# Performance work log

Hardware: AMD Instinct MI355X
Metric: run time of the kernel (lower is better)

## Reference

```python
import jax, jax.numpy as jnp
import numpy as np

D_MODEL = 1024
NUM_HEADS = 16
HEAD_DIM = D_MODEL // NUM_HEADS
B, S = 4, 2048


def setup_inputs() -> dict:
    key = jax.random.key(0)
    ks = jax.random.split(key, 11)
    scale = 1.0 / np.sqrt(D_MODEL)
    inp = {
        "query": jax.random.normal(ks[0], (B, S, D_MODEL), dtype=jnp.float32),
        "key": jax.random.normal(ks[1], (B, S, D_MODEL), dtype=jnp.float32),
        "value": jax.random.normal(ks[2], (B, S, D_MODEL), dtype=jnp.float32),
        "Wq": jax.random.normal(ks[3], (D_MODEL, D_MODEL), dtype=jnp.float32) * scale,
        "bq": jnp.zeros((D_MODEL,), dtype=jnp.float32),
        "Wk": jax.random.normal(ks[4], (D_MODEL, D_MODEL), dtype=jnp.float32) * scale,
        "bk": jnp.zeros((D_MODEL,), dtype=jnp.float32),
        "Wv": jax.random.normal(ks[5], (D_MODEL, D_MODEL), dtype=jnp.float32) * scale,
        "bv": jnp.zeros((D_MODEL,), dtype=jnp.float32),
        "Wo": jax.random.normal(ks[6], (D_MODEL, D_MODEL), dtype=jnp.float32) * scale,
        "bo": jnpp.zeros((D_MODEL,), dtype=jnp.float32) if False else jnp.zeros((D_MODEL,), dtype=jnp.float32),
    }
    return inp


def reference(query, key, value, Wq, bq, Wk, bk, Wv, bv, Wo, bo):
    # Linear projections (torch Linear: x @ W.T + b), split into heads: [B,H,S,Dh]
    def split_heads(x):
        b, s, _ = x.shape
        return x.reshape(b, s, NUM_HEADS, HEAD_DIM).transpose(0, 2, 1, 3)

    q = split_heads(query @ Wq.T + bq)
    k = split_heads(key @ Wk.T + bk)
    v = split_heads(value @ Wv.T + bv)

    # Explicit attention: [B,H,S,S] scores, softmax, AV
    scores = jnp.einsum("bhqd,bhkd->bhqk", q, k) / np.sqrt(HEAD_DIM).astype(np.float32)
    attn = jax.nn.softmax(scores, axis=-1)
    ctx = jnp.einsum("bhqk,bhkd->bhqd", attn, v)

    # Merge heads and output projection
    b = ctx.shape[0]
    ctx = ctx.transpose(0, 2, 1, 3).reshape(b, -1, D_MODEL)
    return ctx @ Wo.T + bo
```

## Files before the change

### kernel.cpp

```cpp
#include <hip/hip_runtime.h>
#include <stdint.h>

#define DMODEL 1024
#define NHEADS 16
#define HDIM   64
#define BB     4
#define SS     2048
#define MM     (BB*SS)
#define QKV_ELEMS ((size_t)8388608)

typedef unsigned short ushort_t;
typedef __bf16    bf16x8  __attribute__((ext_vector_type(8)));
typedef _Float16  half4   __attribute__((ext_vector_type(4)));
typedef _Float16  half2_t __attribute__((ext_vector_type(2)));
typedef float     floatx4 __attribute__((ext_vector_type(4)));

__device__ inline ushort_t f32_to_bf16(float f) {
    union { float f; uint32_t u; } v; v.f = f;
    uint32_t r = v.u + 0x7FFF + ((v.u >> 16) & 1);
    return (ushort_t)(r >> 16);
}
__device__ inline ushort_t f32_to_f16u(float f) {
    union { _Float16 h; ushort_t u; } v; v.h = (_Float16)f; return v.u;
}
__device__ inline half2_t pkrtz(float a, float b) {
    return __builtin_bit_cast(half2_t, __builtin_amdgcn_cvt_pkrtz(a, b));
}
__device__ inline void glds16(const void* g, void* l) {
    __builtin_amdgcn_global_load_lds(
        (const __attribute__((address_space(1))) unsigned int*)g,
        (__attribute__((address_space(3))) unsigned int*)l, 16, 0, 0);
}

__global__ __launch_bounds__(256) void convert_bf16(const float* __restrict__ in,
                                                    ushort_t* __restrict__ out) {
    size_t i = ((size_t)blockIdx.x * 256 + threadIdx.x) * 8;
    float4 a = *(const float4*)&in[i];
    float4 b = *(const float4*)&in[i + 4];
    ushort_t t[8];
    t[0] = f32_to_bf16(a.x); t[1] = f32_to_bf16(a.y);
    t[2] = f32_to_bf16(a.z); t[3] = f32_to_bf16(a.w);
    t[4] = f32_to_bf16(b.x); t[5] = f32_to_bf16(b.y);
    t[6] = f32_to_bf16(b.z); t[7] = f32_to_bf16(b.w);
    *(uint4*)&out[i] = *(uint4*)t;
}

__global__ __launch_bounds__(256) void convert_w3(
    const float* __restrict__ w0, const float* __restrict__ w1, const float* __restrict__ w2,
    ushort_t* __restrict__ o0, ushort_t* __restrict__ o1, ushort_t* __restrict__ o2) {
    const float* src = (blockIdx.y == 0) ? w0 : (blockIdx.y == 1) ? w1 : w2;
    ushort_t*    dst = (blockIdx.y == 0) ? o0 : (blockIdx.y == 1) ? o1 : o2;
    size_t i = ((size_t)blockIdx.x * 256 + threadIdx.x) * 8;
    float4 a = *(const float4*)&src[i];
    float4 b = *(const float4*)&src[i + 4];
    ushort_t t[8];
    t[0] = f32_to_bf16(a.x); t[1] = f32_to_bf16(a.y);
    t[2] = f32_to_bf16(a.z); t[3] = f32_to_bf16(a.w);
    t[4] = f32_to_bf16(b.x); t[5] = f32_to_bf16(b.y);
    t[6] = f32_to_bf16(b.z); t[7] = f32_to_bf16(b.w);
    *(uint4*)&dst[i] = *(uint4*)t;
}

template<int OUT>
__global__ __launch_bounds__(256) void gemm_bf16(
    const ushort_t* __restrict__ A, const ushort_t* __restrict__ W,
    const float* __restrict__ bias, void* __restrict__ O, float scale)
{
    __shared__ ushort_t As[3 * 4096];
    __shared__ ushort_t Bs[3 * 4096];

    const int tid  = threadIdx.x;
    const int lane = tid & 63;
    const int quad = lane >> 4;
    const int l15  = lane & 15;
    const int wid  = tid >> 6;
    const int wr   = wid >> 1, wc = wid & 1;

    const int bid = blockIdx.x;
    const int n0  = ((bid >> 3) & 7) * 128;
    const int m0  = ((bid & 7) + ((bid >> 6) << 3)) * 128;

    floatx4 acc[4][4];
    #pragma unroll
    for (int i = 0; i < 4; i++)
        #pragma unroll
        for (int j = 0; j < 4; j++)
            acc[i][j] = (floatx4){0.f, 0.f, 0.f, 0.f};

    auto stage = [&](int kk, int bufB) {
        #pragma unroll
        for (int j = 0; j < 2; j++) {
            const int p  = tid + j * 256;
            const int ph = p << 4;
            const int lg = ph ^ (((ph >> 7) & 7) << 4);
            const int row = lg >> 6, cc = (lg >> 4) & 3;
            glds16(&A[(size_t)(m0 + row) * DMODEL + kk + cc * 8], (char*)As + bufB + ph);
            glds16(&W[(size_t)(n0 + row) * DMODEL + kk + cc * 8], (char*)Bs + bufB + ph);
        }
    };

    stage(0, 0);
    stage(32, 8192);

    int cbB = 0;
    for (int k0 = 0; k0 < DMODEL; k0 += 32) {
        if (k0 + 32 < DMODEL) asm volatile("s_waitcnt vmcnt(4)" ::: "memory");
        else                  asm volatile("s_waitcnt vmcnt(0)" ::: "memory");
        __builtin_amdgcn_s_barrier();
        __builtin_amdgcn_sched_barrier(0);
        const int k2 = k0 + 64;
        if (k2 < DMODEL) {
            int nbB = cbB + 16384; if (nbB >= 24576) nbB -= 24576;
            stage(k2, nbB);
        }
        bf16x8 af[4], bfv[4];
        #pragma unroll
        for (int i = 0; i < 4; i++) {
            const int r = wr * 64 + i * 16 + l15;
            const int L = (r << 6) | (quad << 4);
            af[i] = *(const bf16x8*)((const char*)As + cbB + (L ^ (((r >> 1) & 7) << 4)));
        }
        #pragma unroll
        for (int j = 0; j < 4; j++) {
            const int r = wc * 64 + j * 16 + l15;
            const int L = (r << 6) | (quad << 4);
            bfv[j] = *(const bf16x8*)((const char*)Bs + cbB + (L ^ (((r >> 1) & 7) << 4)));
        }
        #pragma unroll
        for (int i = 0; i < 4; i++)
            #pragma unroll
            for (int j = 0; j < 4; j++)
                acc[i][j] = __builtin_amdgcn_mfma_f32_16x16x32_bf16(af[i], bfv[j], acc[i][j], 0, 0, 0);
        cbB += 8192; if (cbB == 24576) cbB = 0;
    }

    #pragma unroll
    for (int j = 0; j < 4; j++) {
        const int n = n0 + wc * 64 + j * 16 + l15;
        const float bn = bias[n];
        #pragma unroll
        for (int i = 0; i < 4; i++) {
            #pragma unroll
            for (int r = 0; r < 4; r++) {
                const int m = m0 + wr * 64 + i * 16 + quad * 4 + r;
                float v = (acc[i][j][r] + bn) * scale;
                if (OUT == 0) {
                    const int b = m >> 11, s = m & 2047;
                    const int hh = n >> 6, dh = n & 63;
                    ((ushort_t*)O)[(((size_t)(b * NHEADS + hh)) * SS + s) * HDIM + dh] = f32_to_bf16(v);
                } else if (OUT == 1) {
                    const int b = m >> 11, s = m & 2047;
                    const int hh = n >> 6, dh = n & 63;
                    ((ushort_t*)O)[(((size_t)(b * NHEADS + hh)) * SS + s) * HDIM + dh] = f32_to_f16u(v);
                } else {
                    ((float*)O)[(size_t)m * DMODEL + n] = v;
                }
            }
        }
    }
}

__global__ __launch_bounds__(256, 4) void attn_kernel(
    const ushort_t* __restrict__ Q, const ushort_t* __restrict__ K,
    const ushort_t* __restrict__ V, ushort_t* __restrict__ ctx)
{
    constexpr int LDV = 72;
    constexpr int VOFF = 2 * 4096;
    __shared__ ushort_t smem[2 * 4096 + 2 * 64 * LDV];
    ushort_t* Tr = smem;

    const int tid  = threadIdx.x;
    const int lane = tid & 63;
    const int wid  = tid >> 6;
    const int quad = lane >> 4;
    const int l15  = lane & 15;
    const int bid  = blockIdx.x;
    const int bh   = (bid & 7) * 8 + (bid >> 7);
    const int b    = bh >> 4, h = bh & 15;
    const int q0   = ((bid >> 3) & 15) * 128 + wid * 32;

    const ushort_t* Qb = Q + (size_t)bh * SS * HDIM;
    const ushort_t* Kb = K + (size_t)bh * SS * HDIM;
    const ushort_t* Vb = V + (size_t)bh * SS * HDIM;

    bf16x8 qf[2][2];
    #pragma unroll
    for (int qt = 0; qt < 2; qt++)
        #pragma unroll
        for (int c = 0; c < 2; c++)
            qf[qt][c] = *(const bf16x8*)&Qb[(size_t)(q0 + qt * 16 + l15) * HDIM + c * 32 + quad * 8];

    floatx4 acc[2][4];
    #pragma unroll
    for (int qt = 0; qt < 2; qt++)
        #pragma unroll
        for (int dt = 0; dt < 4; dt++)
            acc[qt][dt] = (floatx4){0.f, 0.f, 0.f, 0.f};
    float lrun[2] = {0.f, 0.f};

    const int kp = tid & 31;
    const int dc = tid >> 5;

    #pragma unroll
    for (int j = 0; j < 2; j++) {
        const int p = tid + j * 256, row = p >> 3, cc = (p & 7) ^ (row & 7);
        glds16(&Kb[(size_t)row * HDIM + cc * 8], &smem[p * 8]);
    }
    {
        ushort_t ua[8], ub[8];
        *(uint4*)ua = *(const uint4*)&Vb[(size_t)(2 * kp) * HDIM + dc * 8];
        *(uint4*)ub = *(const uint4*)&Vb[(size_t)(2 * kp + 1) * HDIM + dc * 8];
        #pragma unroll
        for (int i = 0; i < 8; i++)
            *(uint32_t*)&smem[VOFF + (dc * 8 + i) * LDV + 2 * kp] = (uint32_t)ua[i] | ((uint32_t)ub[i] << 16);
    }

    const half2_t one2 = {(_Float16)1.f, (_Float16)1.f};

    for (int kt = 0; kt < SS; kt += 64) {
        const int cur = ((kt >> 6) & 1);
        const int ko  = cur * 4096;
        const int kon = 4096 - ko;
        const int vo  = VOFF + cur * (64 * LDV);
        const int von = VOFF + (64 * LDV) - cur * (64 * LDV);
        __syncthreads();

        const int ktn = (kt + 64) & (SS - 1);
        #pragma unroll
        for (int j = 0; j < 2; j++) {
            const int p = tid + j * 256, row = p >> 3, cc = (p & 7) ^ (row & 7);
            glds16(&Kb[(size_t)(ktn + row) * HDIM + cc * 8], &smem[kon + p * 8]);
        }
        ushort_t ua[8], ub[8];
        *(uint4*)ua = *(const uint4*)&Vb[(size_t)(ktn + 2 * kp) * HDIM + dc * 8];
        *(uint4*)ub = *(const uint4*)&Vb[(size_t)(ktn + 2 * kp + 1) * HDIM + dc * 8];

        bf16x8 kf[4][2];
        #pragma unroll
        for (int nt = 0; nt < 4; nt++) {
            const int row = nt * 16 + l15;
            #pragma unroll
            for (int c = 0; c < 2; c++) {
                const int pos = (c * 4 + quad) ^ (row & 7);
                kf[nt][c] = *(const bf16x8*)&smem[ko + row * 64 + pos * 8];
            }
        }
        half4 vf[4][4];
        #pragma unroll
        for (int kb = 0; kb < 4; kb++)
            #pragma unroll
            for (int dt = 0; dt < 4; dt++)
                vf[kb][dt] = *(const half4*)&smem[vo + (dt * 16 + l15) * LDV + kb * 16 + quad * 4];

        #pragma unroll
        for (int qt = 0; qt < 2; qt++) {
            floatx4 s[4];
            #pragma unroll
            for (int nt = 0; nt < 4; nt++) {
                floatx4 cz = (floatx4){0.f, 0.f, 0.f, 0.f};
                cz = __builtin_amdgcn_mfma_f32_16x16x32_bf16(kf[nt][0], qf[qt][0], cz, 0, 0, 0);
                cz = __builtin_amdgcn_mfma_f32_16x16x32_bf16(kf[nt][1], qf[qt][1], cz, 0, 0, 0);
                s[nt] = cz;
            }

            float ps = 0.f;
            half4 pf[4];
            #pragma unroll
            for (int nt = 0; nt < 4; nt++) {
                const float p0 = __builtin_amdgcn_exp2f(s[nt][0]);
                const float p1 = __builtin_amdgcn_exp2f(s[nt][1]);
                const float p2 = __builtin_amdgcn_exp2f(s[nt][2]);
                const float p3 = __builtin_amdgcn_exp2f(s[nt][3]);
                const half2_t ha = pkrtz(p0, p1);
                const half2_t hb = pkrtz(p2, p3);
                ps = __builtin_amdgcn_fdot2(ha, one2, ps, false);
                ps = __builtin_amdgcn_fdot2(hb, one2, ps, false);
                union { half4 h4; half2_t h2[2]; } u;
                u.h2[0] = ha; u.h2[1] = hb;
                pf[nt] = u.h4;
            }
            lrun[qt] += ps;

            #pragma unroll
            for (int kb = 0; kb < 4; kb++)
                #pragma unroll
                for (int dt = 0; dt < 4; dt++)
                    acc[qt][dt] = __builtin_amdgcn_mfma_f32_16x16x16f16(vf[kb][dt], pf[kb], acc[qt][dt], 0, 0, 0);
        }

        #pragma unroll
        for (int i = 0; i < 8; i++)
            *(uint32_t*)&smem[von + (dc * 8 + i) * LDV + 2 * kp] = (uint32_t)ua[i] | ((uint32_t)ub[i] << 16);
    }

    float l0 = lrun[0];
    l0 += __shfl_xor(l0, 16); l0 += __shfl_xor(l0, 32);
    float l1 = lrun[1];
    l1 += __shfl_xor(l1, 16); l1 += __shfl_xor(l1, 32);

    __syncthreads();
    const float inv0 = 1.f / l0, inv1 = 1.f / l1;
    ushort_t* Tw = Tr + wid * (32 * LDV);
    #pragma unroll
    for (int qt = 0; qt < 2; qt++) {
        const float inv = qt ? inv1 : inv0;
        #pragma unroll
        for (int dt = 0; dt < 4; dt++)
            #pragma unroll
            for (int r = 0; r < 4; r++)
                Tw[(qt * 16 + l15) * LDV + dt * 16 + quad * 4 + r] = f32_to_bf16(acc[qt][dt][r] * inv);
    }
    const int row = lane >> 1, hf = lane & 1;
    const ushort_t* src = Tw + row * LDV + hf * 32;
    ushort_t* dst = ctx + ((size_t)(b * SS) + q0 + row) * DMODEL + h * HDIM + hf * 32;
    #pragma unroll
    for (int i = 0; i < 4; i++)
        *(uint4*)(dst + i * 8) = *(const uint4*)(src + i * 8);
}

extern "C" void kernel_launch(void* const* d_in, const int* in_sizes, int n_in,
                              void* d_out, int out_size, void* d_ws, size_t ws_size,
                              hipStream_t stream) {
    (void)in_sizes; (void)n_in; (void)out_size; (void)ws_size;
    const float* query = (const float*)d_in[0];
    const float* key_  = (const float*)d_in[1];
    const float* value = (const float*)d_in[2];
    const float* Wq = (const float*)d_in[3];
    const float* bq = (const float*)d_in[4];
    const float* Wk = (const float*)d_in[5];
    const float* bk = (const float*)d_in[6];
    const float* Wv = (const float*)d_in[7];
    const float* bv = (const float*)d_in[8];
    const float* Wo = (const float*)d_in[9];
    const float* bo = (const float*)d_in[10];
    float* out = (float*)d_out;

    ushort_t* tmp = (ushort_t*)d_ws;
    ushort_t* Qw  = tmp + QKV_ELEMS;
    ushort_t* Kw  = Qw + QKV_ELEMS;
    ushort_t* Vw  = Kw + QKV_ELEMS;
    ushort_t* ctx = tmp;
    ushort_t* Wqb = (ushort_t*)d_out;
    ushort_t* Wkb = Wqb + 1048576;
    ushort_t* Wvb = Wkb + 1048576;
    ushort_t* Wob = Qw;

    dim3 blk(256);
    dim3 gg(512);

    hipLaunchKernelGGL(convert_w3, dim3(512, 3), blk, 0, stream, Wq, Wk, Wv, Wqb, Wkb, Wvb);

    hipLaunchKernelGGL(convert_bf16, dim3(4096), blk, 0, stream, query, tmp);
    hipLaunchKernelGGL((gemm_bf16<0>), gg, blk, 0, stream, tmp, Wqb, bq, (void*)Qw, 0.18033688011f);
    hipLaunchKernelGGL(convert_bf16, dim3(4096), blk, 0, stream, key_, tmp);
    hipLaunchKernelGGL((gemm_bf16<0>), gg, blk, 0, stream, tmp, Wkb, bk, (void*)Kw, 1.0f);
    hipLaunchKernelGGL(convert_bf16, dim3(4096), blk, 0, stream, value, tmp);
    hipLaunchKernelGGL((gemm_bf16<1>), gg, blk, 0, stream, tmp, Wvb, bv, (void*)Vw, 1.0f);

    hipLaunchKernelGGL(attn_kernel, dim3(1024), blk, 0, stream, Qw, Kw, Vw, ctx);

    hipLaunchKernelGGL(convert_bf16, dim3(512), blk, 0, stream, Wo, Wob);
    hipLaunchKernelGGL((gemm_bf16<2>), gg, blk, 0, stream, ctx, Wob, bo, (void*)out, 1.0f);
}
```

Before: 367.2 us.

## Fuse fp32-to-bf16 input conversion into a single batched QKV projection GEMM

Replaces three convert+GEMM pairs with one kernel that reads fp32 activations directly, converts them to bf16 in registers while staging into LDS, and processes Q, K and V in a single 1536-block launch. This removes three conversion kernels and their round-trips through the temporary buffer, plus launch overhead. The attention kernel also switches its PV product from 16x16x16 f16 MFMAs to 16x16x32 f16 MFMAs, with a permuted V row mapping so 8-wide LDS reads line up with the larger K dimension. The fp32 A loads are twice the bytes of bf16 and go through registers rather than direct-to-LDS copies, which could raise register pressure or latency.

```diff
diff --git a/kernel.cpp b/kernel.cpp
--- a/kernel.cpp
+++ b/kernel.cpp
@@ -12,6 +12,7 @@
 typedef unsigned short ushort_t;
 typedef __bf16    bf16x8  __attribute__((ext_vector_type(8)));
 typedef _Float16  half4   __attribute__((ext_vector_type(4)));
+typedef _Float16  half8   __attribute__((ext_vector_type(8)));
 typedef _Float16  half2_t __attribute__((ext_vector_type(2)));
 typedef float     floatx4 __attribute__((ext_vector_type(4)));
 
@@ -61,6 +62,140 @@
     *(uint4*)&dst[i] = *(uint4*)t;
 }
 
+__global__ __launch_bounds__(256) void gemm_qkv(
+    const float* __restrict__ Aq, const float* __restrict__ Ak, const float* __restrict__ Av,
+    const ushort_t* __restrict__ Wqp, const ushort_t* __restrict__ Wkp, const ushort_t* __restrict__ Wvp,
+    const float* __restrict__ bq, const float* __restrict__ bk, const float* __restrict__ bv,
+    ushort_t* __restrict__ Oq, ushort_t* __restrict__ Ok, ushort_t* __restrict__ Ov)
+{
+    __shared__ ushort_t As[3 * 4096];
+    __shared__ ushort_t Bs[3 * 4096];
+
+    const int tid  = threadIdx.x;
+    const int lane = tid & 63;
+    const int quad = lane >> 4;
+    const int l15  = lane & 15;
+    const int wid  = tid >> 6;
+    const int wr   = wid >> 1, wc = wid & 1;
+
+    const int bid = blockIdx.x;
+    const int g   = bid >> 9;
+    const int b9  = bid & 511;
+    const int n0  = ((b9 >> 3) & 7) * 128;
+    const int m0  = ((b9 & 7) + ((b9 >> 6) << 3)) * 128;
+
+    const float*    Af   = (g == 0) ? Aq  : (g == 1) ? Ak  : Av;
+    const ushort_t* W    = (g == 0) ? Wqp : (g == 1) ? Wkp : Wvp;
+    const float*    bias = (g == 0) ? bq  : (g == 1) ? bk  : bv;
+    ushort_t*       Oz   = (g == 0) ? Oq  : (g == 1) ? Ok  : Ov;
+    const float     scale = (g == 0) ? 0.18033688011f : 1.0f;
+
+    int rowj[2], ccj[2], phj[2];
+    #pragma unroll
+    for (int j = 0; j < 2; j++) {
+        const int p  = tid + j * 256;
+        const int ph = p << 4;
+        const int lg = ph ^ (((ph >> 7) & 7) << 4);
+        rowj[j] = lg >> 6; ccj[j] = (lg >> 4) & 3; phj[j] = ph;
+    }
+
+    floatx4 acc[4][4];
+    #pragma unroll
+    for (int i = 0; i < 4; i++)
+        #pragma unroll
+        for (int j = 0; j < 4; j++)
+            acc[i][j] = (floatx4){0.f, 0.f, 0.f, 0.f};
+
+    float4 arA[2][2], arB[2][2];
+
+    #pragma unroll
+    for (int j = 0; j < 2; j++) {
+        const float* sA = &Af[(size_t)(m0 + rowj[j]) * DMODEL + ccj[j] * 8];
+        arA[j][0] = *(const float4*)sA; arA[j][1] = *(const float4*)(sA + 4);
+        glds16(&W[(size_t)(n0 + rowj[j]) * DMODEL + ccj[j] * 8], (char*)Bs + phj[j]);
+    }
+    __builtin_amdgcn_sched_barrier(0);
+    #pragma unroll
+    for (int j = 0; j < 2; j++) {
+        const float* sA = &Af[(size_t)(m0 + rowj[j]) * DMODEL + 32 + ccj[j] * 8];
+        arB[j][0] = *(const float4*)sA; arB[j][1] = *(const float4*)(sA + 4);
+        glds16(&W[(size_t)(n0 + rowj[j]) * DMODEL + 32 + ccj[j] * 8], (char*)Bs + 8192 + phj[j]);
+    }
+    __builtin_amdgcn_sched_barrier(0);
+
+    auto tile_body = [&](int kt_, float4 (&ar)[2][2], int cbB_) {
+        if (kt_ + 32 < DMODEL) asm volatile("s_waitcnt vmcnt(6)" ::: "memory");
+        else                   asm volatile("s_waitcnt vmcnt(0)" ::: "memory");
+        #pragma unroll
+        for (int j = 0; j < 2; j++) {
+            ushort_t t8[8];
+            t8[0] = f32_to_bf16(ar[j][0].x); t8[1] = f32_to_bf16(ar[j][0].y);
+            t8[2] = f32_to_bf16(ar[j][0].z); t8[3] = f32_to_bf16(ar[j][0].w);
+            t8[4] = f32_to_bf16(ar[j][1].x); t8[5] = f32_to_bf16(ar[j][1].y);
+            t8[6] = f32_to_bf16(ar[j][1].z); t8[7] = f32_to_bf16(ar[j][1].w);
+            *(uint4*)((char*)As + cbB_ + phj[j]) = *(uint4*)t8;
+        }
+        asm volatile("s_waitcnt lgkmcnt(0)" ::: "memory");
+        __builtin_amdgcn_s_barrier();
+        __builtin_amdgcn_sched_barrier(0);
+        const int k2 = kt_ + 64;
+        if (k2 < DMODEL) {
+            int nbB = cbB_ + 16384; if (nbB >= 24576) nbB -= 24576;
+            #pragma unroll
+            for (int j = 0; j < 2; j++) {
+                const float* sA = &Af[(size_t)(m0 + rowj[j]) * DMODEL + k2 + ccj[j] * 8];
+                ar[j][0] = *(const float4*)sA; ar[j][1] = *(const float4*)(sA + 4);
+                glds16(&W[(size_t)(n0 + rowj[j]) * DMODEL + k2 + ccj[j] * 8], (char*)Bs + nbB + phj[j]);
+            }
+            __builtin_amdgcn_sched_barrier(0);
+        }
+        bf16x8 af[4], bfv[4];
+        #pragma unroll
+        for (int i = 0; i < 4; i++) {
+            const int r = wr * 64 + i * 16 + l15;
+            const int L = (r << 6) | (quad << 4);
+            af[i] = *(const bf16x8*)((const char*)As + cbB_ + (L ^ (((r >> 1) & 7) << 4)));
+        }
+        #pragma unroll
+        for (int j = 0; j < 4; j++) {
+            const int r = wc * 64 + j * 16 + l15;
+            const int L = (r << 6) | (quad << 4);
+            bfv[j] = *(const bf16x8*)((const char*)Bs + cbB_ + (L ^ (((r >> 1) & 7) << 4)));
+        }
+        #pragma unroll
+        for (int i = 0; i < 4; i++)
+            #pragma unroll
+            for (int j = 0; j < 4; j++)
+                acc[i][j] = __builtin_amdgcn_mfma_f32_16x16x32_bf16(af[i], bfv[j], acc[i][j], 0, 0, 0);
+    };
+
+    int cbB = 0;
+    for (int k0 = 0; k0 < DMODEL; k0 += 64) {
+        tile_body(k0, arA, cbB);
+        cbB += 8192; if (cbB == 24576) cbB = 0;
+        tile_body(k0 + 32, arB, cbB);
+        cbB += 8192; if (cbB == 24576) cbB = 0;
+    }
+
+    #pragma unroll
+    for (int j = 0; j < 4; j++) {
+        const int n = n0 + wc * 64 + j * 16 + l15;
+        const float bn = bias[n];
+        #pragma unroll
+        for (int i = 0; i < 4; i++) {
+            #pragma unroll
+            for (int r = 0; r < 4; r++) {
+                const int m = m0 + wr * 64 + i * 16 + quad * 4 + r;
+                const float v = (acc[i][j][r] + bn) * scale;
+                const int bb = m >> 11, s = m & 2047;
+                const int hh = n >> 6, dh = n & 63;
+                Oz[(((size_t)(bb * NHEADS + hh)) * SS + s) * HDIM + dh] =
+                    (g == 2) ? f32_to_f16u(v) : f32_to_bf16(v);
+            }
+        }
+    }
+}
+
 template<int OUT>
 __global__ __launch_bounds__(256) void gemm_bf16(
     const ushort_t* __restrict__ A, const ushort_t* __restrict__ W,
@@ -200,6 +335,8 @@
 
     const int kp = tid & 31;
     const int dc = tid >> 5;
+    const int cvc = 2 * kp;
+    const int vr0 = (cvc & 0x23) | ((cvc & 0x4) << 2) | ((cvc & 0x18) >> 1);
 
     #pragma unroll
     for (int j = 0; j < 2; j++) {
@@ -208,11 +345,11 @@
     }
     {
         ushort_t ua[8], ub[8];
-        *(uint4*)ua = *(const uint4*)&Vb[(size_t)(2 * kp) * HDIM + dc * 8];
-        *(uint4*)ub = *(const uint4*)&Vb[(size_t)(2 * kp + 1) * HDIM + dc * 8];
+        *(uint4*)ua = *(const uint4*)&Vb[(size_t)(vr0) * HDIM + dc * 8];
+        *(uint4*)ub = *(const uint4*)&Vb[(size_t)(vr0 + 1) * HDIM + dc * 8];
         #pragma unroll
         for (int i = 0; i < 8; i++)
-            *(uint32_t*)&smem[VOFF + (dc * 8 + i) * LDV + 2 * kp] = (uint32_t)ua[i] | ((uint32_t)ub[i] << 16);
+            *(uint32_t*)&smem[VOFF + (dc * 8 + i) * LDV + cvc] = (uint32_t)ua[i] | ((uint32_t)ub[i] << 16);
     }
 
     const half2_t one2 = {(_Float16)1.f, (_Float16)1.f};
@@ -232,8 +369,8 @@
             glds16(&Kb[(size_t)(ktn + row) * HDIM + cc * 8], &smem[kon + p * 8]);
         }
         ushort_t ua[8], ub[8];
-        *(uint4*)ua = *(const uint4*)&Vb[(size_t)(ktn + 2 * kp) * HDIM + dc * 8];
-        *(uint4*)ub = *(const uint4*)&Vb[(size_t)(ktn + 2 * kp + 1) * HDIM + dc * 8];
+        *(uint4*)ua = *(const uint4*)&Vb[(size_t)(ktn + vr0) * HDIM + dc * 8];
+        *(uint4*)ub = *(const uint4*)&Vb[(size_t)(ktn + vr0 + 1) * HDIM + dc * 8];
 
         bf16x8 kf[4][2];
         #pragma unroll
@@ -245,12 +382,12 @@
                 kf[nt][c] = *(const bf16x8*)&smem[ko + row * 64 + pos * 8];
             }
         }
-        half4 vf[4][4];
-        #pragma unroll
-        for (int kb = 0; kb < 4; kb++)
+        half8 vf8[2][4];
+        #pragma unroll
+        for (int kb2 = 0; kb2 < 2; kb2++)
             #pragma unroll
             for (int dt = 0; dt < 4; dt++)
-                vf[kb][dt] = *(const half4*)&smem[vo + (dt * 16 + l15) * LDV + kb * 16 + quad * 4];
+                vf8[kb2][dt] = *(const half8*)&smem[vo + (dt * 16 + l15) * LDV + kb2 * 32 + quad * 8];
 
         #pragma unroll
         for (int qt = 0; qt < 2; qt++) {
@@ -264,7 +401,7 @@
             }
 
             float ps = 0.f;
-            half4 pf[4];
+            half2_t ph2[8];
             #pragma unroll
             for (int nt = 0; nt < 4; nt++) {
                 const float p0 = __builtin_amdgcn_exp2f(s[nt][0]);
@@ -275,22 +412,24 @@
                 const half2_t hb = pkrtz(p2, p3);
                 ps = __builtin_amdgcn_fdot2(ha, one2, ps, false);
                 ps = __builtin_amdgcn_fdot2(hb, one2, ps, false);
-                union { half4 h4; half2_t h2[2]; } u;
-                u.h2[0] = ha; u.h2[1] = hb;
-                pf[nt] = u.h4;
+                ph2[nt * 2] = ha; ph2[nt * 2 + 1] = hb;
             }
             lrun[qt] += ps;
 
-            #pragma unroll
-            for (int kb = 0; kb < 4; kb++)
-                #pragma unroll
-                for (int dt = 0; dt < 4; dt++)
-                    acc[qt][dt] = __builtin_amdgcn_mfma_f32_16x16x16f16(vf[kb][dt], pf[kb], acc[qt][dt], 0, 0, 0);
+            union { half2_t h2[4]; half8 h8; } c0, c1;
+            c0.h2[0] = ph2[0]; c0.h2[1] = ph2[1]; c0.h2[2] = ph2[2]; c0.h2[3] = ph2[3];
+            c1.h2[0] = ph2[4]; c1.h2[1] = ph2[5]; c1.h2[2] = ph2[6]; c1.h2[3] = ph2[7];
+
+            #pragma unroll
+            for (int dt = 0; dt < 4; dt++) {
+                acc[qt][dt] = __builtin_amdgcn_mfma_f32_16x16x32_f16(vf8[0][dt], c0.h8, acc[qt][dt], 0, 0, 0);
+                acc[qt][dt] = __builtin_amdgcn_mfma_f32_16x16x32_f16(vf8[1][dt], c1.h8, acc[qt][dt], 0, 0, 0);
+            }
         }
 
         #pragma unroll
         for (int i = 0; i < 8; i++)
-            *(uint32_t*)&smem[von + (dc * 8 + i) * LDV + 2 * kp] = (uint32_t)ua[i] | ((uint32_t)ub[i] << 16);
+            *(uint32_t*)&smem[von + (dc * 8 + i) * LDV + cvc] = (uint32_t)ua[i] | ((uint32_t)ub[i] << 16);
     }
 
     float l0 = lrun[0];
@@ -346,19 +485,14 @@
     ushort_t* Wob = Qw;
 
     dim3 blk(256);
-    dim3 gg(512);
 
     hipLaunchKernelGGL(convert_w3, dim3(512, 3), blk, 0, stream, Wq, Wk, Wv, Wqb, Wkb, Wvb);
 
-    hipLaunchKernelGGL(convert_bf16, dim3(4096), blk, 0, stream, query, tmp);
-    hipLaunchKernelGGL((gemm_bf16<0>), gg, blk, 0, stream, tmp, Wqb, bq, (void*)Qw, 0.18033688011f);
-    hipLaunchKernelGGL(convert_bf16, dim3(4096), blk, 0, stream, key_, tmp);
-    hipLaunchKernelGGL((gemm_bf16<0>), gg, blk, 0, stream, tmp, Wkb, bk, (void*)Kw, 1.0f);
-    hipLaunchKernelGGL(convert_bf16, dim3(4096), blk, 0, stream, value, tmp);
-    hipLaunchKernelGGL((gemm_bf16<1>), gg, blk, 0, stream, tmp, Wvb, bv, (void*)Vw, 1.0f);
+    hipLaunchKernelGGL(gemm_qkv, dim3(1536), blk, 0, stream,
+                       query, key_, value, Wqb, Wkb, Wvb, bq, bk, bv, Qw, Kw, Vw);
 
     hipLaunchKernelGGL(attn_kernel, dim3(1024), blk, 0, stream, Qw, Kw, Vw, ctx);
 
     hipLaunchKernelGGL(convert_bf16, dim3(512), blk, 0, stream, Wo, Wob);
-    hipLaunchKernelGGL((gemm_bf16<2>), gg, blk, 0, stream, ctx, Wob, bo, (void*)out, 1.0f);
-}
+    hipLaunchKernelGGL((gemm_bf16<2>), dim3(512), blk, 0, stream, ctx, Wob, bo, (void*)out, 1.0f);
+}
```

Result: slower. 382.0 us (+4.0%).

## Batch Q and K projection GEMMs into one launch and prioritize MFMA in attention

Applied to the files above, without the earlier changes.

Adds a gemm_qk kernel that runs the Q and K projections in a single 1024-block grid, so one launch fills the GPU better than two 512-block launches. The workspace layout changes to make room: V now lives in the output buffer after the bf16 weights, and ctx and Wo use the scratch slots. The attention kernel also wraps its two MFMA phases in s_setprio(1)/s_setprio(0) to favour matrix issue across waves. In exchange it duplicates the GEMM code, and it relies on the output buffer being large enough to hold the weights plus V until the final GEMM overwrites it.

```diff
diff --git a/kernel.cpp b/kernel.cpp
--- a/kernel.cpp
+++ b/kernel.cpp
@@ -160,6 +160,106 @@
     }
 }
 
+__global__ __launch_bounds__(256) void gemm_qk(
+    const ushort_t* __restrict__ A0, const ushort_t* __restrict__ A1,
+    const ushort_t* __restrict__ W0, const ushort_t* __restrict__ W1,
+    const float* __restrict__ b0, const float* __restrict__ b1,
+    ushort_t* __restrict__ O0, ushort_t* __restrict__ O1, float scale0)
+{
+    __shared__ ushort_t As[3 * 4096];
+    __shared__ ushort_t Bs[3 * 4096];
+
+    const int tid  = threadIdx.x;
+    const int lane = tid & 63;
+    const int quad = lane >> 4;
+    const int l15  = lane & 15;
+    const int wid  = tid >> 6;
+    const int wr   = wid >> 1, wc = wid & 1;
+
+    const int bid = blockIdx.x;
+    const int g   = bid >> 9;
+    const int b9  = bid & 511;
+    const int n0  = ((b9 >> 3) & 7) * 128;
+    const int m0  = ((b9 & 7) + ((b9 >> 6) << 3)) * 128;
+
+    const ushort_t* A    = g ? A1 : A0;
+    const ushort_t* W    = g ? W1 : W0;
+    const float*    bias = g ? b1 : b0;
+    ushort_t*       Oz   = g ? O1 : O0;
+    const float     scale = g ? 1.0f : scale0;
+
+    floatx4 acc[4][4];
+    #pragma unroll
+    for (int i = 0; i < 4; i++)
+        #pragma unroll
+        for (int j = 0; j < 4; j++)
+            acc[i][j] = (floatx4){0.f, 0.f, 0.f, 0.f};
+
+    auto stage = [&](int kk, int bufB) {
+        #pragma unroll
+        for (int j = 0; j < 2; j++) {
+            const int p  = tid + j * 256;
+            const int ph = p << 4;
+            const int lg = ph ^ (((ph >> 7) & 7) << 4);
+            const int row = lg >> 6, cc = (lg >> 4) & 3;
+            glds16(&A[(size_t)(m0 + row) * DMODEL + kk + cc * 8], (char*)As + bufB + ph);
+            glds16(&W[(size_t)(n0 + row) * DMODEL + kk + cc * 8], (char*)Bs + bufB + ph);
+        }
+    };
+
+    stage(0, 0);
+    stage(32, 8192);
+
+    int cbB = 0;
+    for (int k0 = 0; k0 < DMODEL; k0 += 32) {
+        if (k0 + 32 < DMODEL) asm volatile("s_waitcnt vmcnt(4)" ::: "memory");
+        else                  asm volatile("s_waitcnt vmcnt(0)" ::: "memory");
+        __builtin_amdgcn_s_barrier();
+        __builtin_amdgcn_sched_barrier(0);
+        const int k2 = k0 + 64;
+        if (k2 < DMODEL) {
+            int nbB = cbB + 16384; if (nbB >= 24576) nbB -= 24576;
+            stage(k2, nbB);
+        }
+        bf16x8 af[4], bfv[4];
+        #pragma unroll
+        for (int i = 0; i < 4; i++) {
+            const int r = wr * 64 + i * 16 + l15;
+            const int L = (r << 6) | (quad << 4);
+            af[i] = *(const bf16x8*)((const char*)As + cbB + (L ^ (((r >> 1) & 7) << 4)));
+        }
+        #pragma unroll
+        for (int j = 0; j < 4; j++) {
+            const int r = wc * 64 + j * 16 + l15;
+            const int L = (r << 6) | (quad << 4);
+            bfv[j] = *(const bf16x8*)((const char*)Bs + cbB + (L ^ (((r >> 1) & 7) << 4)));
+        }
+        #pragma unroll
+        for (int i = 0; i < 4; i++)
+            #pragma unroll
+            for (int j = 0; j < 4; j++)
+                acc[i][j] = __builtin_amdgcn_mfma_f32_16x16x32_bf16(af[i], bfv[j], acc[i][j], 0, 0, 0);
+        cbB += 8192; if (cbB == 24576) cbB = 0;
+    }
+
+    #pragma unroll
+    for (int j = 0; j < 4; j++) {
+        const int n = n0 + wc * 64 + j * 16 + l15;
+        const float bn = bias[n];
+        #pragma unroll
+        for (int i = 0; i < 4; i++) {
+            #pragma unroll
+            for (int r = 0; r < 4; r++) {
+                const int m = m0 + wr * 64 + i * 16 + quad * 4 + r;
+                const float v = (acc[i][j][r] + bn) * scale;
+                const int bb = m >> 11, s = m & 2047;
+                const int hh = n >> 6, dh = n & 63;
+                Oz[(((size_t)(bb * NHEADS + hh)) * SS + s) * HDIM + dh] = f32_to_bf16(v);
+            }
+        }
+    }
+}
+
 __global__ __launch_bounds__(256, 4) void attn_kernel(
     const ushort_t* __restrict__ Q, const ushort_t* __restrict__ K,
     const ushort_t* __restrict__ V, ushort_t* __restrict__ ctx)
@@ -255,6 +355,7 @@
         #pragma unroll
         for (int qt = 0; qt < 2; qt++) {
             floatx4 s[4];
+            __builtin_amdgcn_s_setprio(1);
             #pragma unroll
             for (int nt = 0; nt < 4; nt++) {
                 floatx4 cz = (floatx4){0.f, 0.f, 0.f, 0.f};
@@ -262,6 +363,7 @@
                 cz = __builtin_amdgcn_mfma_f32_16x16x32_bf16(kf[nt][1], qf[qt][1], cz, 0, 0, 0);
                 s[nt] = cz;
             }
+            __builtin_amdgcn_s_setprio(0);
 
             float ps = 0.f;
             half4 pf[4];
@@ -281,11 +383,13 @@
             }
             lrun[qt] += ps;
 
+            __builtin_amdgcn_s_setprio(1);
             #pragma unroll
             for (int kb = 0; kb < 4; kb++)
                 #pragma unroll
                 for (int dt = 0; dt < 4; dt++)
                     acc[qt][dt] = __builtin_amdgcn_mfma_f32_16x16x16f16(vf[kb][dt], pf[kb], acc[qt][dt], 0, 0, 0);
+            __builtin_amdgcn_s_setprio(0);
         }
 
         #pragma unroll
@@ -335,30 +439,29 @@
     const float* bo = (const float*)d_in[10];
     float* out = (float*)d_out;
 
-    ushort_t* tmp = (ushort_t*)d_ws;
-    ushort_t* Qw  = tmp + QKV_ELEMS;
-    ushort_t* Kw  = Qw + QKV_ELEMS;
-    ushort_t* Vw  = Kw + QKV_ELEMS;
-    ushort_t* ctx = tmp;
+    ushort_t* s0 = (ushort_t*)d_ws;
+    ushort_t* s1 = s0 + QKV_ELEMS;
+    ushort_t* Qw = s1 + QKV_ELEMS;
+    ushort_t* Kw = Qw + QKV_ELEMS;
     ushort_t* Wqb = (ushort_t*)d_out;
     ushort_t* Wkb = Wqb + 1048576;
     ushort_t* Wvb = Wkb + 1048576;
-    ushort_t* Wob = Qw;
+    ushort_t* Vw  = Wvb + 1048576;
 
     dim3 blk(256);
-    dim3 gg(512);
 
     hipLaunchKernelGGL(convert_w3, dim3(512, 3), blk, 0, stream, Wq, Wk, Wv, Wqb, Wkb, Wvb);
 
-    hipLaunchKernelGGL(convert_bf16, dim3(4096), blk, 0, stream, query, tmp);
-    hipLaunchKernelGGL((gemm_bf16<0>), gg, blk, 0, stream, tmp, Wqb, bq, (void*)Qw, 0.18033688011f);
-    hipLaunchKernelGGL(convert_bf16, dim3(4096), blk, 0, stream, key_, tmp);
-    hipLaunchKernelGGL((gemm_bf16<0>), gg, blk, 0, stream, tmp, Wkb, bk, (void*)Kw, 1.0f);
-    hipLaunchKernelGGL(convert_bf16, dim3(4096), blk, 0, stream, value, tmp);
-    hipLaunchKernelGGL((gemm_bf16<1>), gg, blk, 0, stream, tmp, Wvb, bv, (void*)Vw, 1.0f);
-
-    hipLaunchKernelGGL(attn_kernel, dim3(1024), blk, 0, stream, Qw, Kw, Vw, ctx);
-
-    hipLaunchKernelGGL(convert_bf16, dim3(512), blk, 0, stream, Wo, Wob);
-    hipLaunchKernelGGL((gemm_bf16<2>), gg, blk, 0, stream, ctx, Wob, bo, (void*)out, 1.0f);
-}
+    hipLaunchKernelGGL(convert_bf16, dim3(4096), blk, 0, stream, query, s0);
+    hipLaunchKernelGGL(convert_bf16, dim3(4096), blk, 0, stream, key_, s1);
+    hipLaunchKernelGGL(gemm_qk, dim3(1024), blk, 0, stream,
+                       s0, s1, Wqb, Wkb, bq, bk, Qw, Kw, 0.18033688011f);
+
+    hipLaunchKernelGGL(convert_bf16, dim3(4096), blk, 0, stream, value, s0);
+    hipLaunchKernelGGL((gemm_bf16<1>), dim3(512), blk, 0, stream, s0, Wvb, bv, (void*)Vw, 1.0f);
+
+    hipLaunchKernelGGL(attn_kernel, dim3(1024), blk, 0, stream, Qw, Kw, Vw, s1);
+
+    hipLaunchKernelGGL(convert_bf16, dim3(512), blk, 0, stream, Wo, s0);
+    hipLaunchKernelGGL((gemm_bf16<2>), dim3(512), blk, 0, stream, s1, s0, bo, (void*)out, 1.0f);
+}
```

Result: slower. 574.2 us (+56.4%).
